# Kernel tuning notes

Hardware: AMD Instinct MI355X
Metric: run time of the kernel (lower is better)

Reference implementation:

```python
import jax, jax.numpy as jnp
import numpy as np

TTT_LR = 0.01
LN_EPS = 1e-5


def setup_inputs() -> dict:
    key = jax.random.key(0)
    ks = jax.random.split(key, 4)
    B, S, D, DS = 4, 2048, 1024, 64
    sc = 1.0 / np.sqrt(D).astype(np.float32)
    return {
        "x": jax.random.normal(ks[0], (B, S, D), dtype=jnp.float32),
        "Wk": jax.random.normal(ks[1], (DS, D), dtype=jnp.float32) * sc,
        "bk": jnp.zeros((DS,), jnp.float32),
        "Wv": jax.random.normal(ks[2], (D, D), dtype=jnp.float32) * sc,
        "bv": jnp.zeros((D,), jnp.float32),
        "Wq": jax.random.normal(ks[3], (DS, D), dtype=jnp.float32) * sc,
        "bq": jnp.zeros((DS,), jnp.float32),
        "gamma": jnp.ones((D,), jnp.float32),
        "beta": jnp.zeros((D,), jnp.float32),
    }


def reference(x, Wk, bk, Wv, bv, Wq, bq, gamma, beta):
    B, S, D = x.shape
    DS = Wk.shape[0]
    # LayerNorm over last dim
    mu = jnp.mean(x, axis=-1, keepdims=True)
    var = jnp.mean((x - mu) ** 2, axis=-1, keepdims=True)
    h = (x - mu) * jax.lax.rsqrt(var + LN_EPS) * gamma + beta
    # projections: keys/queries (B,S,DS), values (B,S,D)
    keys = jnp.einsum('bsd,ed->bse', h, Wk) + bk
    values = jnp.einsum('bsd,ed->bse', h, Wv) + bv
    queries = jnp.einsum('bsd,ed->bse', h, Wq) + bq

    def step(W, qkv):
        # W: (B, D, DS) fast-weight state
        q_t, k_t, v_t = qkv  # (B,DS), (B,DS), (B,D)
        y_t = jnp.einsum('bds,bs->bd', W, q_t)      # read with query
        pred = jnp.einsum('bds,bs->bd', W, k_t)     # predict with key
        err = pred - v_t                             # (B, D)
        W = W - TTT_LR * err[:, :, None] * k_t[:, None, :]  # rank-1 grad step
        return W, y_t

    W0 = jnp.zeros((B, D, DS), x.dtype)
    # scan over time: inputs as (S, B, ...)
    qs = jnp.swapaxes(queries, 0, 1)
    ks_ = jnp.swapaxes(keys, 0, 1)
    vs = jnp.swapaxes(values, 0, 1)
    _, ys = jax.lax.scan(step, W0, (qs, ks_, vs))   # ys: (S, B, D)
    y = jnp.swapaxes(ys, 0, 1)
    return x + y
```

## Files before the change

### kernel.cpp

```cpp
#include <hip/hip_runtime.h>
#include <hip/hip_bf16.h>

#define TTT_LR 0.01f
#define LN_EPS 1e-5f

#define BB 4
#define SS 2048
#define DD 1024
#define DSZ 64
#define CHUNK 64
#define NC (SS / CHUNK)
#define NCAT 1152
#define NCVT (NCAT * DD / 4 / 256)
#define MiB (1024ull * 1024ull)

typedef __hip_bfloat16 bf16;
typedef __bf16 bf16x8 __attribute__((ext_vector_type(8)));
typedef float f32x4 __attribute__((ext_vector_type(4)));

__device__ __forceinline__ void gload_lds16(const void* g, void* l) {
    __builtin_amdgcn_global_load_lds(
        (const __attribute__((address_space(1))) unsigned int*)g,
        (__attribute__((address_space(3))) unsigned int*)l, 16, 0, 0);
}

__device__ __forceinline__ void barrier_lgkm() {
    asm volatile("s_waitcnt lgkmcnt(0)" ::: "memory");
    __builtin_amdgcn_s_barrier();
    asm volatile("" ::: "memory");
}

__global__ __launch_bounds__(256) void pre_kernel(
    const float* __restrict__ Wk, const float* __restrict__ Wq,
    const float* __restrict__ Wv, bf16* __restrict__ Wcat,
    const float* __restrict__ x, const float* __restrict__ gamma,
    const float* __restrict__ beta, bf16* __restrict__ hb)
{
    __shared__ float wsum[4], wsum2[4];
    const int tid = threadIdx.x;

    if (blockIdx.x < NCVT) {
        const int i = blockIdx.x * 256 + tid;
        const int idx = i * 4;
        const int row = idx >> 10, col = idx & 1023;
        const float* src = (row < 64)  ? (Wk + (size_t)row * DD)
                         : (row < 128) ? (Wq + (size_t)(row - 64) * DD)
                                       : (Wv + (size_t)(row - 128) * DD);
        float4 v = *reinterpret_cast<const float4*>(src + col);
        bf16 h4[4] = {__float2bfloat16(v.x), __float2bfloat16(v.y),
                      __float2bfloat16(v.z), __float2bfloat16(v.w)};
        *reinterpret_cast<ushort4*>(Wcat + idx) = *reinterpret_cast<ushort4*>(h4);
        return;
    }

    const int row = blockIdx.x - NCVT;
    const int lane = tid & 63, wave = tid >> 6;

    float4 v0 = *reinterpret_cast<const float4*>(x + (size_t)row * DD + tid * 4);
    float s = v0.x + v0.y + v0.z + v0.w;
    float s2 = fmaf(v0.x, v0.x, fmaf(v0.y, v0.y, fmaf(v0.z, v0.z, v0.w * v0.w)));
    #pragma unroll
    for (int off = 32; off > 0; off >>= 1) {
        s  += __shfl_down(s, off, 64);
        s2 += __shfl_down(s2, off, 64);
    }
    if (lane == 0) { wsum[wave] = s; wsum2[wave] = s2; }
    __syncthreads();
    s  = wsum[0] + wsum[1] + wsum[2] + wsum[3];
    s2 = wsum2[0] + wsum2[1] + wsum2[2] + wsum2[3];
    const float mu = s * (1.0f / DD);
    const float rs = rsqrtf(s2 * (1.0f / DD) - mu * mu + LN_EPS);

    float4 g  = *reinterpret_cast<const float4*>(gamma + tid * 4);
    float4 be = *reinterpret_cast<const float4*>(beta + tid * 4);
    bf16 h4[4];
    h4[0] = __float2bfloat16((v0.x - mu) * rs * g.x + be.x);
    h4[1] = __float2bfloat16((v0.y - mu) * rs * g.y + be.y);
    h4[2] = __float2bfloat16((v0.z - mu) * rs * g.z + be.z);
    h4[3] = __float2bfloat16((v0.w - mu) * rs * g.w + be.w);
    *reinterpret_cast<ushort4*>(hb + (size_t)row * DD + tid * 4) =
        *reinterpret_cast<ushort4*>(h4);
}

__global__ __launch_bounds__(256) void kqv_kernel(
    const bf16* __restrict__ h, const bf16* __restrict__ Wcat,
    const float* __restrict__ bk, const float* __restrict__ bq,
    const float* __restrict__ bv,
    float* __restrict__ kbuf, float* __restrict__ qbuf, bf16* __restrict__ vbuf16)
{
    __shared__ bf16 Ash[64 * 64];
    __shared__ bf16 Bsh[128 * 64];
    const int tid = threadIdx.x, lane = tid & 63, wave = tid >> 6;
    const int m = lane & 15, quad = lane >> 4;
    const int wr = wave >> 1, wc = wave & 1;

    const int id = blockIdx.x;
    const int tile = (id & 7) * 144 + (id >> 3);
    const int mtile = tile / 9;
    const int ntile = tile % 9;
    const int m0 = mtile * 64;
    const int n0 = ntile * 128;

    const int srow = wave * 8 + (lane >> 3);
    const int scb = lane & 7;

    f32x4 acc[2][4] = {};

    for (int k0 = 0; k0 < DD; k0 += 64) {
        __syncthreads();
        #pragma unroll
        for (int i = 0; i < 2; ++i) {
            const int row = i * 32 + srow;
            const int g16 = scb ^ (row & 7);
            gload_lds16(h    + (size_t)(m0 + row) * DD + k0 + g16 * 8,
                        (char*)Ash + (size_t)(i * 32 + wave * 8) * 128);
        }
        #pragma unroll
        for (int i = 0; i < 4; ++i) {
            const int row = i * 32 + srow;
            const int g16 = scb ^ (row & 7);
            gload_lds16(Wcat + (size_t)(n0 + row) * DD + k0 + g16 * 8,
                        (char*)Bsh + (size_t)(i * 32 + wave * 8) * 128);
        }
        __syncthreads();
        #pragma unroll
        for (int ks = 0; ks < 2; ++ks) {
            bf16x8 af[2], bfr[4];
            #pragma unroll
            for (int mt = 0; mt < 2; ++mt) {
                const int row = wr * 32 + mt * 16 + m;
                const int kb = (ks * 4 + quad) ^ (row & 7);
                af[mt] = *reinterpret_cast<const bf16x8*>(&Ash[row * 64 + kb * 8]);
            }
            #pragma unroll
            for (int nt = 0; nt < 4; ++nt) {
                const int row = wc * 64 + nt * 16 + m;
                const int kb = (ks * 4 + quad) ^ (row & 7);
                bfr[nt] = *reinterpret_cast<const bf16x8*>(&Bsh[row * 64 + kb * 8]);
            }
            #pragma unroll
            for (int mt = 0; mt < 2; ++mt)
                #pragma unroll
                for (int nt = 0; nt < 4; ++nt)
                    acc[mt][nt] = __builtin_amdgcn_mfma_f32_16x16x32_bf16(
                        af[mt], bfr[nt], acc[mt][nt], 0, 0, 0);
        }
    }

    #pragma unroll
    for (int nt = 0; nt < 4; ++nt) {
        const int n = n0 + wc * 64 + nt * 16 + m;
        if (n < 64) {
            const float bias = bk[n];
            #pragma unroll
            for (int mt = 0; mt < 2; ++mt) {
                const int row = m0 + wr * 32 + mt * 16 + quad * 4;
                #pragma unroll
                for (int r = 0; r < 4; ++r)
                    kbuf[(size_t)(row + r) * DSZ + n] = acc[mt][nt][r] + bias;
            }
        } else if (n < 128) {
            const float bias = bq[n - 64];
            #pragma unroll
            for (int mt = 0; mt < 2; ++mt) {
                const int row = m0 + wr * 32 + mt * 16 + quad * 4;
                #pragma unroll
                for (int r = 0; r < 4; ++r)
                    qbuf[(size_t)(row + r) * DSZ + (n - 64)] = acc[mt][nt][r] + bias;
            }
        } else {
            const float bias = bv[n - 128];
            #pragma unroll
            for (int mt = 0; mt < 2; ++mt) {
                const int row = m0 + wr * 32 + mt * 16 + quad * 4;
                #pragma unroll
                for (int r = 0; r < 4; ++r)
                    vbuf16[(size_t)(row + r) * DD + (n - 128)] =
                        __float2bfloat16(acc[mt][nt][r] + bias);
            }
        }
    }
}

__global__ __launch_bounds__(256) void prep_kernel(
    const float* __restrict__ kbuf, const float* __restrict__ qbuf,
    bf16* __restrict__ Tb16, bf16* __restrict__ Wb16,
    bf16* __restrict__ AMb16, bf16* __restrict__ Qtb16)
{
    __shared__ bf16 K16[64 * 72];
    __shared__ bf16 Kt16[64 * 72];
    __shared__ bf16 Q16[64 * 72];
    __shared__ bf16 Astl[64 * 72];
    __shared__ bf16 Minv16[64 * 72];
    __shared__ bf16 MinvT16[64 * 72];
    __shared__ bf16 BnegT[64 * 72];
    __shared__ __align__(16) float Gf[64 * 68];
    __shared__ __align__(16) float MfT[64 * 68];

    const int c = blockIdx.x, b = blockIdx.y;
    const int tid = threadIdx.x, lane = tid & 63, w = tid >> 6;
    const int m = lane & 15, quad = lane >> 4;
    const float* kp = kbuf + ((size_t)b * SS + c * 64) * DSZ;
    const float* qp = qbuf + ((size_t)b * SS + c * 64) * DSZ;
    const size_t cb = ((size_t)b * NC + c) * 4096;

    #pragma unroll
    for (int it = 0; it < 4; ++it) {
        const int f4 = tid + it * 256;
        const int t = f4 >> 4;
        const int s = (f4 & 15) * 4;
        float4 kv = *reinterpret_cast<const float4*>(kp + t * DSZ + s);
        float4 qv = *reinterpret_cast<const float4*>(qp + t * DSZ + s);
        bf16 kb4[4] = {__float2bfloat16(kv.x), __float2bfloat16(kv.y),
                       __float2bfloat16(kv.z), __float2bfloat16(kv.w)};
        bf16 qb4[4] = {__float2bfloat16(qv.x), __float2bfloat16(qv.y),
                       __float2bfloat16(qv.z), __float2bfloat16(qv.w)};
        *reinterpret_cast<ushort4*>(&K16[t * 72 + s]) = *reinterpret_cast<ushort4*>(kb4);
        *reinterpret_cast<ushort4*>(&Q16[t * 72 + s]) = *reinterpret_cast<ushort4*>(qb4);
        #pragma unroll
        for (int i = 0; i < 4; ++i) Kt16[(s + i) * 72 + t] = kb4[i];
    }
    #pragma unroll
    for (int i = tid; i < 64 * 68; i += 256) MfT[i] = 0.f;
    __syncthreads();

    bf16x8 afK[2], afQ[2], bfK[4][2];
    #pragma unroll
    for (int ks = 0; ks < 2; ++ks) {
        afK[ks] = *reinterpret_cast<const bf16x8*>(&K16[(w * 16 + m) * 72 + ks * 32 + quad * 8]);
        afQ[ks] = *reinterpret_cast<const bf16x8*>(&Q16[(w * 16 + m) * 72 + ks * 32 + quad * 8]);
        #pragma unroll
        for (int nt = 0; nt < 4; ++nt)
            bfK[nt][ks] = *reinterpret_cast<const bf16x8*>(&K16[(nt * 16 + m) * 72 + ks * 32 + quad * 8]);
    }
    f32x4 gacc[4] = {}, aacc[4] = {};
    #pragma unroll
    for (int ks = 0; ks < 2; ++ks)
        #pragma unroll
        for (int nt = 0; nt < 4; ++nt) {
            gacc[nt] = __builtin_amdgcn_mfma_f32_16x16x32_bf16(afK[ks], bfK[nt][ks], gacc[nt], 0, 0, 0);
            aacc[nt] = __builtin_amdgcn_mfma_f32_16x16x32_bf16(afQ[ks], bfK[nt][ks], aacc[nt], 0, 0, 0);
        }
    #pragma unroll
    for (int nt = 0; nt < 4; ++nt)
        #pragma unroll
        for (int r = 0; r < 4; ++r) {
            const int t = w * 16 + quad * 4 + r, j = nt * 16 + m;
            Gf[t * 68 + j] = TTT_LR * gacc[nt][r];
            Astl[t * 72 + j] = __float2bfloat16(j < t ? aacc[nt][r] : 0.f);
        }
    __syncthreads();

    if (tid < 64) {
        for (int t = 0; t < 64; ++t) {
            float a0 = 0.f, a1 = 0.f, a2 = 0.f, a3 = 0.f;
            #pragma unroll
            for (int i4 = 0; i4 < 16; ++i4) {
                const float4 g4 = *reinterpret_cast<const float4*>(&Gf[t * 68 + i4 * 4]);
                const float4 m4 = *reinterpret_cast<const float4*>(&MfT[tid * 68 + i4 * 4]);
                a0 = fmaf(g4.x, m4.x, a0);
                a1 = fmaf(g4.y, m4.y, a1);
                a2 = fmaf(g4.z, m4.z, a2);
                a3 = fmaf(g4.w, m4.w, a3);
            }
            MfT[tid * 68 + t] = ((t == tid) ? 1.f : 0.f) - ((a0 + a1) + (a2 + a3));
        }
    }
    __syncthreads();

    #pragma unroll
    for (int it = 0; it < 16; ++it) {
        const int e = tid + it * 256;
        const int t = e >> 6, j = e & 63;
        const bf16 vb = __float2bfloat16(TTT_LR * MfT[j * 68 + t]);
        Minv16[t * 72 + j] = vb;
        MinvT16[j * 72 + t] = vb;
    }
    __syncthreads();

    bf16x8 afM[2], afA[2], afKt[2], bfKt[4][2], bfMt[4][2];
    #pragma unroll
    for (int ks = 0; ks < 2; ++ks) {
        afM[ks]  = *reinterpret_cast<const bf16x8*>(&Minv16[(w * 16 + m) * 72 + ks * 32 + quad * 8]);
        afA[ks]  = *reinterpret_cast<const bf16x8*>(&Astl[(w * 16 + m) * 72 + ks * 32 + quad * 8]);
        afKt[ks] = *reinterpret_cast<const bf16x8*>(&Kt16[(w * 16 + m) * 72 + ks * 32 + quad * 8]);
        #pragma unroll
        for (int nt = 0; nt < 4; ++nt) {
            bfKt[nt][ks] = *reinterpret_cast<const bf16x8*>(&Kt16[(nt * 16 + m) * 72 + ks * 32 + quad * 8]);
            bfMt[nt][ks] = *reinterpret_cast<const bf16x8*>(&MinvT16[(nt * 16 + m) * 72 + ks * 32 + quad * 8]);
        }
    }
    f32x4 bacc[4] = {};
    #pragma unroll
    for (int ks = 0; ks < 2; ++ks)
        #pragma unroll
        for (int nt = 0; nt < 4; ++nt)
            bacc[nt] = __builtin_amdgcn_mfma_f32_16x16x32_bf16(afM[ks], bfKt[nt][ks], bacc[nt], 0, 0, 0);
    #pragma unroll
    for (int nt = 0; nt < 4; ++nt)
        #pragma unroll
        for (int r = 0; r < 4; ++r) {
            const int t = w * 16 + quad * 4 + r, s = nt * 16 + m;
            BnegT[s * 72 + t] = __float2bfloat16(-bacc[nt][r]);
        }
    __syncthreads();

    f32x4 qtacc[4], amacc[4] = {}, tacc[4] = {}, wacc[4] = {};
    #pragma unroll
    for (int nt = 0; nt < 4; ++nt)
        #pragma unroll
        for (int r = 0; r < 4; ++r)
            qtacc[nt][r] = qp[(w * 16 + quad * 4 + r) * DSZ + nt * 16 + m];
    #pragma unroll
    for (int ks = 0; ks < 2; ++ks)
        #pragma unroll
        for (int nt = 0; nt < 4; ++nt) {
            const bf16x8 bfBn = *reinterpret_cast<const bf16x8*>(
                &BnegT[(nt * 16 + m) * 72 + ks * 32 + quad * 8]);
            qtacc[nt] = __builtin_amdgcn_mfma_f32_16x16x32_bf16(afA[ks], bfBn, qtacc[nt], 0, 0, 0);
            amacc[nt] = __builtin_amdgcn_mfma_f32_16x16x32_bf16(afA[ks], bfMt[nt][ks], amacc[nt], 0, 0, 0);
            tacc[nt]  = __builtin_amdgcn_mfma_f32_16x16x32_bf16(afKt[ks], bfBn, tacc[nt], 0, 0, 0);
            wacc[nt]  = __builtin_amdgcn_mfma_f32_16x16x32_bf16(afKt[ks], bfMt[nt][ks], wacc[nt], 0, 0, 0);
        }
    #pragma unroll
    for (int nt = 0; nt < 4; ++nt)
        #pragma unroll
        for (int r = 0; r < 4; ++r) {
            const int row = w * 16 + quad * 4 + r, col = nt * 16 + m;
            Qtb16[cb + row * 64 + col] = __float2bfloat16(qtacc[nt][r]);
            AMb16[cb + row * 64 + col] = __float2bfloat16(amacc[nt][r]);
            Tb16[cb + row * 64 + col]  = __float2bfloat16(tacc[nt][r]);
            Wb16[cb + row * 64 + col]  = __float2bfloat16(wacc[nt][r]);
        }
}

struct MRegs { bf16x8 T0, T1, W0, W1, A0, A1, Q0, Q1; };
struct VRegs {
    alignas(8) unsigned short va[4], vb[4];
    float xld[4];
};

__global__ __launch_bounds__(256) void scan2_kernel(
    const bf16* __restrict__ Tb16, const bf16* __restrict__ Wb16,
    const bf16* __restrict__ AMb16, const bf16* __restrict__ Qtb16,
    const bf16* __restrict__ v16, const float* __restrict__ x,
    float* __restrict__ out)
{
    __shared__ bf16 Zsh[2][16][72];
    __shared__ bf16 Vsh[2][16][72];
    const int id = blockIdx.x;
    const int tile = (id & 7) * 32 + (id >> 3);
    const int b = tile >> 6, dblk = tile & 63;
    const int tid = threadIdx.x, lane = tid & 63, w = tid >> 6;
    const int m = lane & 15, quad = lane >> 4;
    const int d0 = dblk * 16;
    const int arow = w * 16 + m;
    const int trow = w * 16 + quad * 4;

    const bool vact = tid < 128;
    const int vj2 = (tid & 31) * 2;
    const int vd = (tid >> 5) * 4;

    f32x4 zacc = {0.f, 0.f, 0.f, 0.f};
    for (int i = tid; i < 16 * 72; i += 256)
        (&Zsh[0][0][0])[i] = __float2bfloat16(0.f);

    auto load_m = [&](int c, MRegs& R) {
        const size_t cb = ((size_t)b * NC + c) * 4096;
        R.T0 = *reinterpret_cast<const bf16x8*>(Tb16 + cb + arow * 64 + quad * 8);
        R.T1 = *reinterpret_cast<const bf16x8*>(Tb16 + cb + arow * 64 + 32 + quad * 8);
        R.W0 = *reinterpret_cast<const bf16x8*>(Wb16 + cb + arow * 64 + quad * 8);
        R.W1 = *reinterpret_cast<const bf16x8*>(Wb16 + cb + arow * 64 + 32 + quad * 8);
        R.A0 = *reinterpret_cast<const bf16x8*>(AMb16 + cb + arow * 64 + quad * 8);
        R.A1 = *reinterpret_cast<const bf16x8*>(AMb16 + cb + arow * 64 + 32 + quad * 8);
        R.Q0 = *reinterpret_cast<const bf16x8*>(Qtb16 + cb + arow * 64 + quad * 8);
        R.Q1 = *reinterpret_cast<const bf16x8*>(Qtb16 + cb + arow * 64 + 32 + quad * 8);
    };

    auto load_v = [&](int c, VRegs& V) {
        const size_t rowbase = (size_t)b * SS + (size_t)c * 64;
        if (vact) {
            *reinterpret_cast<uint2*>(V.va) = *reinterpret_cast<const uint2*>(
                v16 + (rowbase + vj2) * DD + d0 + vd);
            *reinterpret_cast<uint2*>(V.vb) = *reinterpret_cast<const uint2*>(
                v16 + (rowbase + vj2 + 1) * DD + d0 + vd);
        }
        const size_t gbase = (rowbase + trow) * DD + d0 + m;
        #pragma unroll
        for (int r = 0; r < 4; ++r) V.xld[r] = x[gbase + (size_t)r * DD];
    };

    auto stage_v = [&](const VRegs& V, int buf) {
        if (vact) {
            #pragma unroll
            for (int i = 0; i < 4; ++i) {
                const unsigned int pack =
                    (unsigned int)V.va[i] | ((unsigned int)V.vb[i] << 16);
                *reinterpret_cast<unsigned int*>(&Vsh[buf][vd + i][vj2]) = pack;
            }
        }
    };

    auto compute = [&](const MRegs& R, const VRegs& V, int c, int buf) {
        const bf16x8 z0 = *reinterpret_cast<const bf16x8*>(&Zsh[buf][m][quad * 8]);
        const bf16x8 z1 = *reinterpret_cast<const bf16x8*>(&Zsh[buf][m][32 + quad * 8]);
        const bf16x8 v0 = *reinterpret_cast<const bf16x8*>(&Vsh[buf][m][quad * 8]);
        const bf16x8 v1 = *reinterpret_cast<const bf16x8*>(&Vsh[buf][m][32 + quad * 8]);

        zacc = __builtin_amdgcn_mfma_f32_16x16x32_bf16(R.T0, z0, zacc, 0, 0, 0);
        zacc = __builtin_amdgcn_mfma_f32_16x16x32_bf16(R.T1, z1, zacc, 0, 0, 0);
        zacc = __builtin_amdgcn_mfma_f32_16x16x32_bf16(R.W0, v0, zacc, 0, 0, 0);
        zacc = __builtin_amdgcn_mfma_f32_16x16x32_bf16(R.W1, v1, zacc, 0, 0, 0);

        alignas(8) bf16 zb[4];
        #pragma unroll
        for (int r = 0; r < 4; ++r) zb[r] = __float2bfloat16(zacc[r]);
        *reinterpret_cast<uint2*>(&Zsh[buf ^ 1][m][trow]) =
            *reinterpret_cast<uint2*>(zb);

        f32x4 y = {0.f, 0.f, 0.f, 0.f};
        y = __builtin_amdgcn_mfma_f32_16x16x32_bf16(R.Q0, z0, y, 0, 0, 0);
        y = __builtin_amdgcn_mfma_f32_16x16x32_bf16(R.Q1, z1, y, 0, 0, 0);
        y = __builtin_amdgcn_mfma_f32_16x16x32_bf16(R.A0, v0, y, 0, 0, 0);
        y = __builtin_amdgcn_mfma_f32_16x16x32_bf16(R.A1, v1, y, 0, 0, 0);

        const size_t gbase = ((size_t)b * SS + (size_t)c * 64 + trow) * DD + d0 + m;
        #pragma unroll
        for (int r = 0; r < 4; ++r)
            out[gbase + (size_t)r * DD] = V.xld[r] + y[r];
    };

    VRegs V0, V1;
    MRegs M0, M1;
    load_v(0, V0);
    load_v(1, V1);
    load_m(0, M0);
    for (int c = 0; c < NC; c += 2) {
        stage_v(V0, 0);
        barrier_lgkm();
        load_m(c + 1, M1);
        compute(M0, V0, c, 0);
        if (c + 2 < NC) load_v(c + 2, V0);

        stage_v(V1, 1);
        barrier_lgkm();
        if (c + 2 < NC) load_m(c + 2, M0);
        compute(M1, V1, c + 1, 1);
        if (c + 3 < NC) load_v(c + 3, V1);
    }
}

extern "C" void kernel_launch(void* const* d_in, const int* in_sizes, int n_in,
                              void* d_out, int out_size, void* d_ws, size_t ws_size,
                              hipStream_t stream)
{
    const float* x     = (const float*)d_in[0];
    const float* Wk    = (const float*)d_in[1];
    const float* bk    = (const float*)d_in[2];
    const float* Wv    = (const float*)d_in[3];
    const float* bv    = (const float*)d_in[4];
    const float* Wq    = (const float*)d_in[5];
    const float* bq    = (const float*)d_in[6];
    const float* gamma = (const float*)d_in[7];
    const float* beta  = (const float*)d_in[8];

    char* ws = (char*)d_ws;
    const size_t WCAT_B = (size_t)NCAT * DD * 2;
    bf16*  hb    = (bf16*)ws;
    bf16*  Tb16  = (bf16*)(ws + 0 * MiB);
    bf16*  Qtb16 = (bf16*)(ws + 1 * MiB);
    bf16*  Wb16  = (bf16*)(ws + 2 * MiB);
    bf16*  AMb16 = (bf16*)(ws + 3 * MiB);
    bf16*  Wcat  = (bf16*)(ws + 16 * MiB);
    float* kbuf  = (float*)(ws + 16 * MiB + WCAT_B);
    float* qbuf  = (float*)(ws + 18 * MiB + WCAT_B);
    bf16*  v16   = (bf16*)(ws + 20 * MiB + WCAT_B);

    pre_kernel<<<NCVT + BB * SS, 256, 0, stream>>>(
        Wk, Wq, Wv, Wcat, x, gamma, beta, hb);
    kqv_kernel<<<dim3(1152), 256, 0, stream>>>(
        hb, Wcat, bk, bq, bv, kbuf, qbuf, v16);
    prep_kernel<<<dim3(NC, BB), 256, 0, stream>>>(
        kbuf, qbuf, Tb16, Wb16, AMb16, Qtb16);
    scan2_kernel<<<dim3(256), 256, 0, stream>>>(
        Tb16, Wb16, AMb16, Qtb16, v16, x, (float*)d_out);
}
```

Baseline: 197.4 us.

## Split scan into Z-recurrence and Y-output warp groups with triple-buffered state

The scan kernel now runs 512 threads split into two roles. Four waves carry only the serial chunk-state recurrence (Z update). The other four waves, one chunk behind, compute the outputs y and the residual add, reading Z from a triple-buffered shared array. V is now loaded straight into MFMA fragments with strided scalar 2-byte loads instead of going through LDS. This moves output work and the x/out traffic off the serial critical path, at the cost of more uncoalesced global loads and barriers across twice as many waves.

```diff
diff --git a/kernel.cpp b/kernel.cpp
--- a/kernel.cpp
+++ b/kernel.cpp
@@ -334,120 +334,128 @@
         }
 }
 
-struct MRegs { bf16x8 T0, T1, W0, W1, A0, A1, Q0, Q1; };
-struct VRegs {
-    alignas(8) unsigned short va[4], vb[4];
-    float xld[4];
-};
-
-__global__ __launch_bounds__(256) void scan2_kernel(
+struct MZr { bf16x8 T0, T1, W0, W1; };
+struct MYr { bf16x8 Q0, Q1, A0, A1; };
+
+__global__ __launch_bounds__(512) void scan2_kernel(
     const bf16* __restrict__ Tb16, const bf16* __restrict__ Wb16,
     const bf16* __restrict__ AMb16, const bf16* __restrict__ Qtb16,
     const bf16* __restrict__ v16, const float* __restrict__ x,
     float* __restrict__ out)
 {
-    __shared__ bf16 Zsh[2][16][72];
-    __shared__ bf16 Vsh[2][16][72];
+    __shared__ bf16 Zsh[3][16][72];
     const int id = blockIdx.x;
     const int tile = (id & 7) * 32 + (id >> 3);
     const int b = tile >> 6, dblk = tile & 63;
-    const int tid = threadIdx.x, lane = tid & 63, w = tid >> 6;
+    const int tid = threadIdx.x, lane = tid & 63, wv = tid >> 6;
+    const bool zg = wv < 4;
+    const int w4 = wv & 3;
     const int m = lane & 15, quad = lane >> 4;
     const int d0 = dblk * 16;
-    const int arow = w * 16 + m;
-    const int trow = w * 16 + quad * 4;
-
-    const bool vact = tid < 128;
-    const int vj2 = (tid & 31) * 2;
-    const int vd = (tid >> 5) * 4;
-
-    f32x4 zacc = {0.f, 0.f, 0.f, 0.f};
-    for (int i = tid; i < 16 * 72; i += 256)
+    const int arow = w4 * 16 + m;
+    const int trow = w4 * 16 + quad * 4;
+
+    for (int i = tid; i < 16 * 72; i += 512)
         (&Zsh[0][0][0])[i] = __float2bfloat16(0.f);
 
-    auto load_m = [&](int c, MRegs& R) {
+    auto load_mz = [&](int c, MZr& R) {
         const size_t cb = ((size_t)b * NC + c) * 4096;
         R.T0 = *reinterpret_cast<const bf16x8*>(Tb16 + cb + arow * 64 + quad * 8);
         R.T1 = *reinterpret_cast<const bf16x8*>(Tb16 + cb + arow * 64 + 32 + quad * 8);
         R.W0 = *reinterpret_cast<const bf16x8*>(Wb16 + cb + arow * 64 + quad * 8);
         R.W1 = *reinterpret_cast<const bf16x8*>(Wb16 + cb + arow * 64 + 32 + quad * 8);
+    };
+    auto load_my = [&](int c, MYr& R) {
+        const size_t cb = ((size_t)b * NC + c) * 4096;
+        R.Q0 = *reinterpret_cast<const bf16x8*>(Qtb16 + cb + arow * 64 + quad * 8);
+        R.Q1 = *reinterpret_cast<const bf16x8*>(Qtb16 + cb + arow * 64 + 32 + quad * 8);
         R.A0 = *reinterpret_cast<const bf16x8*>(AMb16 + cb + arow * 64 + quad * 8);
         R.A1 = *reinterpret_cast<const bf16x8*>(AMb16 + cb + arow * 64 + 32 + quad * 8);
-        R.Q0 = *reinterpret_cast<const bf16x8*>(Qtb16 + cb + arow * 64 + quad * 8);
-        R.Q1 = *reinterpret_cast<const bf16x8*>(Qtb16 + cb + arow * 64 + 32 + quad * 8);
-    };
-
-    auto load_v = [&](int c, VRegs& V) {
-        const size_t rowbase = (size_t)b * SS + (size_t)c * 64;
-        if (vact) {
-            *reinterpret_cast<uint2*>(V.va) = *reinterpret_cast<const uint2*>(
-                v16 + (rowbase + vj2) * DD + d0 + vd);
-            *reinterpret_cast<uint2*>(V.vb) = *reinterpret_cast<const uint2*>(
-                v16 + (rowbase + vj2 + 1) * DD + d0 + vd);
-        }
-        const size_t gbase = (rowbase + trow) * DD + d0 + m;
-        #pragma unroll
-        for (int r = 0; r < 4; ++r) V.xld[r] = x[gbase + (size_t)r * DD];
-    };
-
-    auto stage_v = [&](const VRegs& V, int buf) {
-        if (vact) {
-            #pragma unroll
-            for (int i = 0; i < 4; ++i) {
-                const unsigned int pack =
-                    (unsigned int)V.va[i] | ((unsigned int)V.vb[i] << 16);
-                *reinterpret_cast<unsigned int*>(&Vsh[buf][vd + i][vj2]) = pack;
-            }
-        }
-    };
-
-    auto compute = [&](const MRegs& R, const VRegs& V, int c, int buf) {
-        const bf16x8 z0 = *reinterpret_cast<const bf16x8*>(&Zsh[buf][m][quad * 8]);
-        const bf16x8 z1 = *reinterpret_cast<const bf16x8*>(&Zsh[buf][m][32 + quad * 8]);
-        const bf16x8 v0 = *reinterpret_cast<const bf16x8*>(&Vsh[buf][m][quad * 8]);
-        const bf16x8 v1 = *reinterpret_cast<const bf16x8*>(&Vsh[buf][m][32 + quad * 8]);
-
-        zacc = __builtin_amdgcn_mfma_f32_16x16x32_bf16(R.T0, z0, zacc, 0, 0, 0);
-        zacc = __builtin_amdgcn_mfma_f32_16x16x32_bf16(R.T1, z1, zacc, 0, 0, 0);
-        zacc = __builtin_amdgcn_mfma_f32_16x16x32_bf16(R.W0, v0, zacc, 0, 0, 0);
-        zacc = __builtin_amdgcn_mfma_f32_16x16x32_bf16(R.W1, v1, zacc, 0, 0, 0);
-
+    };
+    auto load_vf = [&](int c, bf16x8& f0, bf16x8& f1) {
+        const bf16* src = v16 + ((size_t)b * SS + (size_t)c * 64) * DD + d0 + m;
+        union { bf16x8 v; unsigned short u[8]; } A, B;
+        #pragma unroll
+        for (int j = 0; j < 8; ++j) {
+            A.u[j] = *reinterpret_cast<const unsigned short*>(src + (size_t)(quad * 8 + j) * DD);
+            B.u[j] = *reinterpret_cast<const unsigned short*>(src + (size_t)(32 + quad * 8 + j) * DD);
+        }
+        f0 = A.v; f1 = B.v;
+    };
+    auto load_x = [&](int c, float* xs) {
+        const size_t gbase = ((size_t)b * SS + (size_t)c * 64 + trow) * DD + d0 + m;
+        #pragma unroll
+        for (int r = 0; r < 4; ++r) xs[r] = x[gbase + (size_t)r * DD];
+    };
+
+    f32x4 zacc = {0.f, 0.f, 0.f, 0.f};
+    MZr mz[2]; MYr my[2];
+    bf16x8 vz0[4], vz1[4], vy0[4], vy1[4];
+    float xs[4][4];
+
+    if (zg) {
+        load_mz(0, mz[0]);
+        load_vf(0, vz0[0], vz1[0]);
+        load_vf(1, vz0[1], vz1[1]);
+    } else {
+        load_x(0, xs[0]);
+        load_vf(0, vy0[0], vy1[0]);
+    }
+
+    auto zbody = [&](int p, MZr& Mc, MZr& Mn,
+                     const bf16x8& v0, const bf16x8& v1, bf16x8& lv0, bf16x8& lv1) {
+        if (p + 1 < NC) load_mz(p + 1, Mn);
+        if (p + 2 < NC) load_vf(p + 2, lv0, lv1);
+        const int pb = p % 3, pn = (p + 1) % 3;
+        const bf16x8 z0 = *reinterpret_cast<const bf16x8*>(&Zsh[pb][m][quad * 8]);
+        const bf16x8 z1 = *reinterpret_cast<const bf16x8*>(&Zsh[pb][m][32 + quad * 8]);
+        zacc = __builtin_amdgcn_mfma_f32_16x16x32_bf16(Mc.T0, z0, zacc, 0, 0, 0);
+        zacc = __builtin_amdgcn_mfma_f32_16x16x32_bf16(Mc.T1, z1, zacc, 0, 0, 0);
+        zacc = __builtin_amdgcn_mfma_f32_16x16x32_bf16(Mc.W0, v0, zacc, 0, 0, 0);
+        zacc = __builtin_amdgcn_mfma_f32_16x16x32_bf16(Mc.W1, v1, zacc, 0, 0, 0);
         alignas(8) bf16 zb[4];
         #pragma unroll
         for (int r = 0; r < 4; ++r) zb[r] = __float2bfloat16(zacc[r]);
-        *reinterpret_cast<uint2*>(&Zsh[buf ^ 1][m][trow]) =
-            *reinterpret_cast<uint2*>(zb);
-
-        f32x4 y = {0.f, 0.f, 0.f, 0.f};
-        y = __builtin_amdgcn_mfma_f32_16x16x32_bf16(R.Q0, z0, y, 0, 0, 0);
-        y = __builtin_amdgcn_mfma_f32_16x16x32_bf16(R.Q1, z1, y, 0, 0, 0);
-        y = __builtin_amdgcn_mfma_f32_16x16x32_bf16(R.A0, v0, y, 0, 0, 0);
-        y = __builtin_amdgcn_mfma_f32_16x16x32_bf16(R.A1, v1, y, 0, 0, 0);
-
-        const size_t gbase = ((size_t)b * SS + (size_t)c * 64 + trow) * DD + d0 + m;
-        #pragma unroll
-        for (int r = 0; r < 4; ++r)
-            out[gbase + (size_t)r * DD] = V.xld[r] + y[r];
-    };
-
-    VRegs V0, V1;
-    MRegs M0, M1;
-    load_v(0, V0);
-    load_v(1, V1);
-    load_m(0, M0);
-    for (int c = 0; c < NC; c += 2) {
-        stage_v(V0, 0);
+        *reinterpret_cast<uint2*>(&Zsh[pn][m][trow]) = *reinterpret_cast<uint2*>(zb);
+    };
+
+    auto ybody = [&](int p, MYr& Mc, MYr& Ml, const float* xc, float* xl,
+                     const bf16x8& v0, const bf16x8& v1, bf16x8& lv0, bf16x8& lv1) {
+        if (p < NC) load_my(p, Ml);
+        if (p + 1 < NC) { load_x(p + 1, xl); load_vf(p + 1, lv0, lv1); }
+        const int c = p - 1;
+        if (c >= 0) {
+            const int cbuf = c % 3;
+            const bf16x8 z0 = *reinterpret_cast<const bf16x8*>(&Zsh[cbuf][m][quad * 8]);
+            const bf16x8 z1 = *reinterpret_cast<const bf16x8*>(&Zsh[cbuf][m][32 + quad * 8]);
+            f32x4 y = {0.f, 0.f, 0.f, 0.f};
+            y = __builtin_amdgcn_mfma_f32_16x16x32_bf16(Mc.Q0, z0, y, 0, 0, 0);
+            y = __builtin_amdgcn_mfma_f32_16x16x32_bf16(Mc.Q1, z1, y, 0, 0, 0);
+            y = __builtin_amdgcn_mfma_f32_16x16x32_bf16(Mc.A0, v0, y, 0, 0, 0);
+            y = __builtin_amdgcn_mfma_f32_16x16x32_bf16(Mc.A1, v1, y, 0, 0, 0);
+            const size_t gbase = ((size_t)b * SS + (size_t)c * 64 + trow) * DD + d0 + m;
+            #pragma unroll
+            for (int r = 0; r < 4; ++r)
+                out[gbase + (size_t)r * DD] = xc[r] + y[r];
+        }
+    };
+
+    for (int p = 0; p < NC; p += 4) {
         barrier_lgkm();
-        load_m(c + 1, M1);
-        compute(M0, V0, c, 0);
-        if (c + 2 < NC) load_v(c + 2, V0);
-
-        stage_v(V1, 1);
+        if (zg) zbody(p,     mz[0], mz[1], vz0[0], vz1[0], vz0[2], vz1[2]);
+        else    ybody(p,     my[1], my[0], xs[3], xs[1], vy0[3], vy1[3], vy0[1], vy1[1]);
         barrier_lgkm();
-        if (c + 2 < NC) load_m(c + 2, M0);
-        compute(M1, V1, c + 1, 1);
-        if (c + 3 < NC) load_v(c + 3, V1);
-    }
+        if (zg) zbody(p + 1, mz[1], mz[0], vz0[1], vz1[1], vz0[3], vz1[3]);
+        else    ybody(p + 1, my[0], my[1], xs[0], xs[2], vy0[0], vy1[0], vy0[2], vy1[2]);
+        barrier_lgkm();
+        if (zg) zbody(p + 2, mz[0], mz[1], vz0[2], vz1[2], vz0[0], vz1[0]);
+        else    ybody(p + 2, my[1], my[0], xs[1], xs[3], vy0[1], vy1[1], vy0[3], vy1[3]);
+        barrier_lgkm();
+        if (zg) zbody(p + 3, mz[1], mz[0], vz0[3], vz1[3], vz0[1], vz1[1]);
+        else    ybody(p + 3, my[0], my[1], xs[2], xs[0], vy0[2], vy1[2], vy0[0], vy1[0]);
+    }
+    barrier_lgkm();
+    if (!zg) ybody(NC, my[1], my[0], xs[3], xs[1], vy0[3], vy1[3], vy0[1], vy1[1]);
 }
 
 extern "C" void kernel_launch(void* const* d_in, const int* in_sizes, int n_in,
@@ -482,6 +490,6 @@
         hb, Wcat, bk, bq, bv, kbuf, qbuf, v16);
     prep_kernel<<<dim3(NC, BB), 256, 0, stream>>>(
         kbuf, qbuf, Tb16, Wb16, AMb16, Qtb16);
-    scan2_kernel<<<dim3(256), 256, 0, stream>>>(
+    scan2_kernel<<<dim3(256), 512, 0, stream>>>(
         Tb16, Wb16, AMb16, Qtb16, v16, x, (float*)d_out);
 }
```

Measured after the change: 213.0 us. 1.08x slower.

## Compose chunk transition matrices in pairs to halve sequential scan steps

Applied to the files above, without the earlier changes.

Adds a prep2 kernel that composes each pair of consecutive 64-step chunk transitions (T, W, Q, AM) into combined pair matrices (U, P, R, S). The scan kernel then advances the recurrent state once per two chunks, halving the serial dependency chain and the number of barriers. In exchange it spends an extra kernel launch and more memory traffic on precomputed matrices, uses more registers per thread, and adds bf16 rounding error from composing matrices.

```diff
diff --git a/kernel.cpp b/kernel.cpp
--- a/kernel.cpp
+++ b/kernel.cpp
@@ -10,6 +10,7 @@
 #define DSZ 64
 #define CHUNK 64
 #define NC (SS / CHUNK)
+#define NP (NC / 2)
 #define NCAT 1152
 #define NCVT (NCAT * DD / 4 / 256)
 #define MiB (1024ull * 1024ull)
@@ -334,20 +335,91 @@
         }
 }
 
-struct MRegs { bf16x8 T0, T1, W0, W1, A0, A1, Q0, Q1; };
-struct VRegs {
+__global__ __launch_bounds__(256) void prep2_kernel(
+    const bf16* __restrict__ Tb16, const bf16* __restrict__ Wb16,
+    const bf16* __restrict__ Qtb16,
+    bf16* __restrict__ Ub, bf16* __restrict__ Pb,
+    bf16* __restrict__ Rb, bf16* __restrict__ Sb)
+{
+    __shared__ bf16 T0T[64 * 72];
+    __shared__ bf16 W0T[64 * 72];
+    const int p = blockIdx.x, b = blockIdx.y;
+    const int tid = threadIdx.x, lane = tid & 63, w = tid >> 6;
+    const int m = lane & 15, quad = lane >> 4;
+    const size_t cb0 = ((size_t)b * NC + 2 * p) * 4096;
+    const size_t cb1 = ((size_t)b * NC + 2 * p + 1) * 4096;
+    const size_t pb  = ((size_t)b * NP + p) * 4096;
+
+    #pragma unroll
+    for (int it = 0; it < 2; ++it) {
+        const int idx = tid + it * 256;
+        const int row = idx >> 3;
+        const int c8 = (idx & 7) * 8;
+        union { bf16x8 v; unsigned short u[8]; } tv, wv;
+        tv.v = *reinterpret_cast<const bf16x8*>(Tb16 + cb0 + row * 64 + c8);
+        wv.v = *reinterpret_cast<const bf16x8*>(Wb16 + cb0 + row * 64 + c8);
+        #pragma unroll
+        for (int j = 0; j < 8; ++j) {
+            *reinterpret_cast<unsigned short*>(&T0T[(c8 + j) * 72 + row]) = tv.u[j];
+            *reinterpret_cast<unsigned short*>(&W0T[(c8 + j) * 72 + row]) = wv.u[j];
+        }
+    }
+    __syncthreads();
+
+    const int arow = w * 16 + m;
+    bf16x8 afT1[2], afQ1[2];
+    #pragma unroll
+    for (int ks = 0; ks < 2; ++ks) {
+        afT1[ks] = *reinterpret_cast<const bf16x8*>(Tb16  + cb1 + arow * 64 + ks * 32 + quad * 8);
+        afQ1[ks] = *reinterpret_cast<const bf16x8*>(Qtb16 + cb1 + arow * 64 + ks * 32 + quad * 8);
+    }
+    f32x4 uacc[4] = {}, pacc[4] = {}, racc[4] = {}, sacc[4] = {};
+    #pragma unroll
+    for (int ks = 0; ks < 2; ++ks)
+        #pragma unroll
+        for (int nt = 0; nt < 4; ++nt) {
+            const bf16x8 bT = *reinterpret_cast<const bf16x8*>(&T0T[(nt * 16 + m) * 72 + ks * 32 + quad * 8]);
+            const bf16x8 bW = *reinterpret_cast<const bf16x8*>(&W0T[(nt * 16 + m) * 72 + ks * 32 + quad * 8]);
+            uacc[nt] = __builtin_amdgcn_mfma_f32_16x16x32_bf16(afT1[ks], bT, uacc[nt], 0, 0, 0);
+            pacc[nt] = __builtin_amdgcn_mfma_f32_16x16x32_bf16(afT1[ks], bW, pacc[nt], 0, 0, 0);
+            racc[nt] = __builtin_amdgcn_mfma_f32_16x16x32_bf16(afQ1[ks], bT, racc[nt], 0, 0, 0);
+            sacc[nt] = __builtin_amdgcn_mfma_f32_16x16x32_bf16(afQ1[ks], bW, sacc[nt], 0, 0, 0);
+        }
+    #pragma unroll
+    for (int nt = 0; nt < 4; ++nt)
+        #pragma unroll
+        for (int r = 0; r < 4; ++r) {
+            const int row = w * 16 + quad * 4 + r, col = nt * 16 + m;
+            const size_t o = (size_t)row * 64 + col;
+            const float u  = uacc[nt][r] + __bfloat162float(Tb16[cb0 + o])
+                                          + __bfloat162float(Tb16[cb1 + o]);
+            const float pp = pacc[nt][r] + __bfloat162float(Wb16[cb0 + o]);
+            const float rr = racc[nt][r] + __bfloat162float(Qtb16[cb1 + o]);
+            Ub[pb + o] = __float2bfloat16(u);
+            Pb[pb + o] = __float2bfloat16(pp);
+            Rb[pb + o] = __float2bfloat16(rr);
+            Sb[pb + o] = __float2bfloat16(sacc[nt][r]);
+        }
+}
+
+struct PairM {
+    bf16x8 U0, U1, P0, P1, Wn0, Wn1, Q0, Q1, A0, A1, R0, R1, S0, S1, B0, B1;
+};
+struct PairV {
     alignas(8) unsigned short va[4], vb[4];
-    float xld[4];
+    float xA[4], xB[4];
 };
 
 __global__ __launch_bounds__(256) void scan2_kernel(
-    const bf16* __restrict__ Tb16, const bf16* __restrict__ Wb16,
-    const bf16* __restrict__ AMb16, const bf16* __restrict__ Qtb16,
+    const bf16* __restrict__ Ub, const bf16* __restrict__ Pb,
+    const bf16* __restrict__ Rb, const bf16* __restrict__ Sb,
+    const bf16* __restrict__ Wb16, const bf16* __restrict__ AMb16,
+    const bf16* __restrict__ Qtb16,
     const bf16* __restrict__ v16, const float* __restrict__ x,
     float* __restrict__ out)
 {
     __shared__ bf16 Zsh[2][16][72];
-    __shared__ bf16 Vsh[2][16][72];
+    __shared__ bf16 Vsh[2][2][16][72];
     const int id = blockIdx.x;
     const int tile = (id & 7) * 32 + (id >> 3);
     const int b = tile >> 6, dblk = tile & 63;
@@ -357,96 +429,115 @@
     const int arow = w * 16 + m;
     const int trow = w * 16 + quad * 4;
 
-    const bool vact = tid < 128;
-    const int vj2 = (tid & 31) * 2;
-    const int vd = (tid >> 5) * 4;
+    const int t2 = tid & 127;
+    const int csel = tid >> 7;
+    const int vj2 = (t2 & 31) * 2;
+    const int vd = (t2 >> 5) * 4;
 
     f32x4 zacc = {0.f, 0.f, 0.f, 0.f};
     for (int i = tid; i < 16 * 72; i += 256)
         (&Zsh[0][0][0])[i] = __float2bfloat16(0.f);
 
-    auto load_m = [&](int c, MRegs& R) {
-        const size_t cb = ((size_t)b * NC + c) * 4096;
-        R.T0 = *reinterpret_cast<const bf16x8*>(Tb16 + cb + arow * 64 + quad * 8);
-        R.T1 = *reinterpret_cast<const bf16x8*>(Tb16 + cb + arow * 64 + 32 + quad * 8);
-        R.W0 = *reinterpret_cast<const bf16x8*>(Wb16 + cb + arow * 64 + quad * 8);
-        R.W1 = *reinterpret_cast<const bf16x8*>(Wb16 + cb + arow * 64 + 32 + quad * 8);
-        R.A0 = *reinterpret_cast<const bf16x8*>(AMb16 + cb + arow * 64 + quad * 8);
-        R.A1 = *reinterpret_cast<const bf16x8*>(AMb16 + cb + arow * 64 + 32 + quad * 8);
-        R.Q0 = *reinterpret_cast<const bf16x8*>(Qtb16 + cb + arow * 64 + quad * 8);
-        R.Q1 = *reinterpret_cast<const bf16x8*>(Qtb16 + cb + arow * 64 + 32 + quad * 8);
+    auto load_pair = [&](int p, PairM& M, PairV& V) {
+        const int c0 = 2 * p, c1 = 2 * p + 1;
+        const size_t pbb = ((size_t)b * NP + p) * 4096;
+        const size_t cb0 = ((size_t)b * NC + c0) * 4096;
+        const size_t cb1 = ((size_t)b * NC + c1) * 4096;
+        M.U0  = *reinterpret_cast<const bf16x8*>(Ub    + pbb + arow * 64 + quad * 8);
+        M.U1  = *reinterpret_cast<const bf16x8*>(Ub    + pbb + arow * 64 + 32 + quad * 8);
+        M.P0  = *reinterpret_cast<const bf16x8*>(Pb    + pbb + arow * 64 + quad * 8);
+        M.P1  = *reinterpret_cast<const bf16x8*>(Pb    + pbb + arow * 64 + 32 + quad * 8);
+        M.Wn0 = *reinterpret_cast<const bf16x8*>(Wb16  + cb1 + arow * 64 + quad * 8);
+        M.Wn1 = *reinterpret_cast<const bf16x8*>(Wb16  + cb1 + arow * 64 + 32 + quad * 8);
+        M.Q0  = *reinterpret_cast<const bf16x8*>(Qtb16 + cb0 + arow * 64 + quad * 8);
+        M.Q1  = *reinterpret_cast<const bf16x8*>(Qtb16 + cb0 + arow * 64 + 32 + quad * 8);
+        M.A0  = *reinterpret_cast<const bf16x8*>(AMb16 + cb0 + arow * 64 + quad * 8);
+        M.A1  = *reinterpret_cast<const bf16x8*>(AMb16 + cb0 + arow * 64 + 32 + quad * 8);
+        M.R0  = *reinterpret_cast<const bf16x8*>(Rb    + pbb + arow * 64 + quad * 8);
+        M.R1  = *reinterpret_cast<const bf16x8*>(Rb    + pbb + arow * 64 + 32 + quad * 8);
+        M.S0  = *reinterpret_cast<const bf16x8*>(Sb    + pbb + arow * 64 + quad * 8);
+        M.S1  = *reinterpret_cast<const bf16x8*>(Sb    + pbb + arow * 64 + 32 + quad * 8);
+        M.B0  = *reinterpret_cast<const bf16x8*>(AMb16 + cb1 + arow * 64 + quad * 8);
+        M.B1  = *reinterpret_cast<const bf16x8*>(AMb16 + cb1 + arow * 64 + 32 + quad * 8);
+        const int cv = csel ? c1 : c0;
+        const size_t vrow = (size_t)b * SS + (size_t)cv * 64;
+        *reinterpret_cast<uint2*>(V.va) = *reinterpret_cast<const uint2*>(
+            v16 + (vrow + vj2) * DD + d0 + vd);
+        *reinterpret_cast<uint2*>(V.vb) = *reinterpret_cast<const uint2*>(
+            v16 + (vrow + vj2 + 1) * DD + d0 + vd);
+        const size_t g0 = ((size_t)b * SS + (size_t)c0 * 64 + trow) * DD + d0 + m;
+        const size_t g1 = ((size_t)b * SS + (size_t)c1 * 64 + trow) * DD + d0 + m;
+        #pragma unroll
+        for (int r = 0; r < 4; ++r) {
+            V.xA[r] = x[g0 + (size_t)r * DD];
+            V.xB[r] = x[g1 + (size_t)r * DD];
+        }
     };
 
-    auto load_v = [&](int c, VRegs& V) {
-        const size_t rowbase = (size_t)b * SS + (size_t)c * 64;
-        if (vact) {
-            *reinterpret_cast<uint2*>(V.va) = *reinterpret_cast<const uint2*>(
-                v16 + (rowbase + vj2) * DD + d0 + vd);
-            *reinterpret_cast<uint2*>(V.vb) = *reinterpret_cast<const uint2*>(
-                v16 + (rowbase + vj2 + 1) * DD + d0 + vd);
-        }
-        const size_t gbase = (rowbase + trow) * DD + d0 + m;
-        #pragma unroll
-        for (int r = 0; r < 4; ++r) V.xld[r] = x[gbase + (size_t)r * DD];
+    auto stage_v = [&](const PairV& V, int buf) {
+        #pragma unroll
+        for (int i = 0; i < 4; ++i) {
+            const unsigned int pack =
+                (unsigned int)V.va[i] | ((unsigned int)V.vb[i] << 16);
+            *reinterpret_cast<unsigned int*>(&Vsh[buf][csel][vd + i][vj2]) = pack;
+        }
     };
 
-    auto stage_v = [&](const VRegs& V, int buf) {
-        if (vact) {
-            #pragma unroll
-            for (int i = 0; i < 4; ++i) {
-                const unsigned int pack =
-                    (unsigned int)V.va[i] | ((unsigned int)V.vb[i] << 16);
-                *reinterpret_cast<unsigned int*>(&Vsh[buf][vd + i][vj2]) = pack;
-            }
-        }
-    };
-
-    auto compute = [&](const MRegs& R, const VRegs& V, int c, int buf) {
+    auto compute = [&](const PairM& M, const PairV& V, int p, int buf) {
+        const int c0 = 2 * p, c1 = 2 * p + 1;
         const bf16x8 z0 = *reinterpret_cast<const bf16x8*>(&Zsh[buf][m][quad * 8]);
         const bf16x8 z1 = *reinterpret_cast<const bf16x8*>(&Zsh[buf][m][32 + quad * 8]);
-        const bf16x8 v0 = *reinterpret_cast<const bf16x8*>(&Vsh[buf][m][quad * 8]);
-        const bf16x8 v1 = *reinterpret_cast<const bf16x8*>(&Vsh[buf][m][32 + quad * 8]);
-
-        zacc = __builtin_amdgcn_mfma_f32_16x16x32_bf16(R.T0, z0, zacc, 0, 0, 0);
-        zacc = __builtin_amdgcn_mfma_f32_16x16x32_bf16(R.T1, z1, zacc, 0, 0, 0);
-        zacc = __builtin_amdgcn_mfma_f32_16x16x32_bf16(R.W0, v0, zacc, 0, 0, 0);
-        zacc = __builtin_amdgcn_mfma_f32_16x16x32_bf16(R.W1, v1, zacc, 0, 0, 0);
-
+        const bf16x8 a0 = *reinterpret_cast<const bf16x8*>(&Vsh[buf][0][m][quad * 8]);
+        const bf16x8 a1 = *reinterpret_cast<const bf16x8*>(&Vsh[buf][0][m][32 + quad * 8]);
+        const bf16x8 b0 = *reinterpret_cast<const bf16x8*>(&Vsh[buf][1][m][quad * 8]);
+        const bf16x8 b1 = *reinterpret_cast<const bf16x8*>(&Vsh[buf][1][m][32 + quad * 8]);
+
+        zacc = __builtin_amdgcn_mfma_f32_16x16x32_bf16(M.U0, z0, zacc, 0, 0, 0);
+        zacc = __builtin_amdgcn_mfma_f32_16x16x32_bf16(M.U1, z1, zacc, 0, 0, 0);
+        zacc = __builtin_amdgcn_mfma_f32_16x16x32_bf16(M.P0, a0, zacc, 0, 0, 0);
+        zacc = __builtin_amdgcn_mfma_f32_16x16x32_bf16(M.P1, a1, zacc, 0, 0, 0);
+        zacc = __builtin_amdgcn_mfma_f32_16x16x32_bf16(M.Wn0, b0, zacc, 0, 0, 0);
+        zacc = __builtin_amdgcn_mfma_f32_16x16x32_bf16(M.Wn1, b1, zacc, 0, 0, 0);
         alignas(8) bf16 zb[4];
         #pragma unroll
         for (int r = 0; r < 4; ++r) zb[r] = __float2bfloat16(zacc[r]);
         *reinterpret_cast<uint2*>(&Zsh[buf ^ 1][m][trow]) =
             *reinterpret_cast<uint2*>(zb);
 
-        f32x4 y = {0.f, 0.f, 0.f, 0.f};
-        y = __builtin_amdgcn_mfma_f32_16x16x32_bf16(R.Q0, z0, y, 0, 0, 0);
-        y = __builtin_amdgcn_mfma_f32_16x16x32_bf16(R.Q1, z1, y, 0, 0, 0);
-        y = __builtin_amdgcn_mfma_f32_16x16x32_bf16(R.A0, v0, y, 0, 0, 0);
-        y = __builtin_amdgcn_mfma_f32_16x16x32_bf16(R.A1, v1, y, 0, 0, 0);
-
-        const size_t gbase = ((size_t)b * SS + (size_t)c * 64 + trow) * DD + d0 + m;
-        #pragma unroll
-        for (int r = 0; r < 4; ++r)
-            out[gbase + (size_t)r * DD] = V.xld[r] + y[r];
+        f32x4 y0 = {0.f, 0.f, 0.f, 0.f};
+        y0 = __builtin_amdgcn_mfma_f32_16x16x32_bf16(M.Q0, z0, y0, 0, 0, 0);
+        y0 = __builtin_amdgcn_mfma_f32_16x16x32_bf16(M.Q1, z1, y0, 0, 0, 0);
+        y0 = __builtin_amdgcn_mfma_f32_16x16x32_bf16(M.A0, a0, y0, 0, 0, 0);
+        y0 = __builtin_amdgcn_mfma_f32_16x16x32_bf16(M.A1, a1, y0, 0, 0, 0);
+        f32x4 y1 = {0.f, 0.f, 0.f, 0.f};
+        y1 = __builtin_amdgcn_mfma_f32_16x16x32_bf16(M.R0, z0, y1, 0, 0, 0);
+        y1 = __builtin_amdgcn_mfma_f32_16x16x32_bf16(M.R1, z1, y1, 0, 0, 0);
+        y1 = __builtin_amdgcn_mfma_f32_16x16x32_bf16(M.S0, a0, y1, 0, 0, 0);
+        y1 = __builtin_amdgcn_mfma_f32_16x16x32_bf16(M.S1, a1, y1, 0, 0, 0);
+        y1 = __builtin_amdgcn_mfma_f32_16x16x32_bf16(M.B0, b0, y1, 0, 0, 0);
+        y1 = __builtin_amdgcn_mfma_f32_16x16x32_bf16(M.B1, b1, y1, 0, 0, 0);
+
+        const size_t g0 = ((size_t)b * SS + (size_t)c0 * 64 + trow) * DD + d0 + m;
+        const size_t g1 = ((size_t)b * SS + (size_t)c1 * 64 + trow) * DD + d0 + m;
+        #pragma unroll
+        for (int r = 0; r < 4; ++r) {
+            out[g0 + (size_t)r * DD] = V.xA[r] + y0[r];
+            out[g1 + (size_t)r * DD] = V.xB[r] + y1[r];
+        }
     };
 
-    VRegs V0, V1;
-    MRegs M0, M1;
-    load_v(0, V0);
-    load_v(1, V1);
-    load_m(0, M0);
-    for (int c = 0; c < NC; c += 2) {
+    PairV V0, V1;
+    PairM M0, M1;
+    load_pair(0, M0, V0);
+    for (int p = 0; p < NP; p += 2) {
         stage_v(V0, 0);
         barrier_lgkm();
-        load_m(c + 1, M1);
-        compute(M0, V0, c, 0);
-        if (c + 2 < NC) load_v(c + 2, V0);
-
+        load_pair(p + 1, M1, V1);
+        compute(M0, V0, p, 0);
         stage_v(V1, 1);
         barrier_lgkm();
-        if (c + 2 < NC) load_m(c + 2, M0);
-        compute(M1, V1, c + 1, 1);
-        if (c + 3 < NC) load_v(c + 3, V1);
+        if (p + 2 < NP) load_pair(p + 2, M0, V0);
+        compute(M1, V1, p + 1, 1);
     }
 }
 
@@ -471,6 +562,10 @@
     bf16*  Qtb16 = (bf16*)(ws + 1 * MiB);
     bf16*  Wb16  = (bf16*)(ws + 2 * MiB);
     bf16*  AMb16 = (bf16*)(ws + 3 * MiB);
+    bf16*  Ub    = (bf16*)(ws + 4 * MiB);
+    bf16*  Pb    = (bf16*)(ws + 4 * MiB + 512 * 1024);
+    bf16*  Rb    = (bf16*)(ws + 5 * MiB);
+    bf16*  Sb    = (bf16*)(ws + 5 * MiB + 512 * 1024);
     bf16*  Wcat  = (bf16*)(ws + 16 * MiB);
     float* kbuf  = (float*)(ws + 16 * MiB + WCAT_B);
     float* qbuf  = (float*)(ws + 18 * MiB + WCAT_B);
@@ -482,6 +577,8 @@
         hb, Wcat, bk, bq, bv, kbuf, qbuf, v16);
     prep_kernel<<<dim3(NC, BB), 256, 0, stream>>>(
         kbuf, qbuf, Tb16, Wb16, AMb16, Qtb16);
+    prep2_kernel<<<dim3(NP, BB), 256, 0, stream>>>(
+        Tb16, Wb16, Qtb16, Ub, Pb, Rb, Sb);
     scan2_kernel<<<dim3(256), 256, 0, stream>>>(
-        Tb16, Wb16, AMb16, Qtb16, v16, x, (float*)d_out);
-}
+        Ub, Pb, Rb, Sb, Wb16, AMb16, Qtb16, v16, x, (float*)d_out);
+}
```

Result: slower. 205.0 us (+3.8%).
